# Kernel tuning notes

Hardware: AMD Instinct MI355X
Metric: run time of the kernel (lower is better)

The kernel has to match this reference:

```python
import jax, jax.numpy as jnp
import numpy as np

H = W = 20
NVARS = 4          # n_predictor_vars
NK = 12            # n_conv2d_kernels
NF = NK + NVARS + 1  # 17 augmented channels (conv + original + time)
SIGLEN = NF + NF * NF  # 306, depth-2 signature length
T_END = 1.0        # self.T in the module


def setup_inputs() -> dict:
    key = jax.random.key(0)
    ks = jax.random.split(key, 8)
    B, T = 64, 96
    x = jax.random.normal(ks[0], (B, T, NVARS, H, W), dtype=jnp.float32)
    conv_w = jax.random.normal(ks[1], (NK, NVARS, 3, 3), dtype=jnp.float32) * 0.1
    conv_b = jax.random.normal(ks[2], (NK,), dtype=jnp.float32) * 0.01
    d_in = SIGLEN * H * W  # 122400

    def lin(k, fan_in, fan_out):
        return jax.random.normal(k, (fan_in, fan_out), dtype=jnp.float32) / np.float32(np.sqrt(fan_in))

    w1, b1 = lin(ks[3], d_in, 32), jnp.zeros((32,), jnp.float32)
    w2, b2 = lin(ks[4], 32, 32), jnp.zeros((32,), jnp.float32)
    w3, b3 = lin(ks[5], 32, 32), jnp.zeros((32,), jnp.float32)
    w4, b4 = lin(ks[6], 32, 1), jnp.zeros((1,), jnp.float32)
    return {"x": x, "conv_w": conv_w, "conv_b": conv_b,
            "w1": w1, "b1": b1, "w2": w2, "b2": b2,
            "w3": w3, "b3": b3, "w4": w4, "b4": b4}


def reference(x, conv_w, conv_b, w1, b1, w2, b2, w3, b3, w4, b4):
    B, T = x.shape[0], x.shape[1]
    # Batched conv over all timesteps at once (the torch code loops over t).
    xi = x.reshape(B * T, NVARS, H, W)
    y = jax.lax.conv_general_dilated(
        xi, conv_w, window_strides=(1, 1), padding='SAME',
        dimension_numbers=('NCHW', 'OIHW', 'NCHW'))
    y = y + conv_b[None, :, None, None]
    y = y.reshape(B, T, NK, H, W)
    # Dropout3d is identity in eval mode.
    # Augment: [conv features, original values, time channel] along channel dim.
    tch = jnp.linspace(0.0, T_END, T, dtype=x.dtype).reshape(1, T, 1, 1, 1)
    tch = jnp.broadcast_to(tch, (B, T, 1, H, W))
    feat = jnp.concatenate([y, x, tch], axis=2)        # (B, T, NF, H, W)
    path = jnp.transpose(feat, (0, 3, 4, 1, 2))        # (B, H, W, T, NF)
    # Depth-2 path signature (Chen closed form):
    # level1 = sum dx; level2 = sum_{i<j} dx_i (x) dx_j + 0.5 sum_i dx_i (x) dx_i
    dx = path[..., 1:, :] - path[..., :-1, :]          # (B,H,W,T-1,NF)
    csum = jnp.cumsum(dx, axis=-2)                     # inclusive prefix sums
    lvl1 = csum[..., -1, :]                            # (B,H,W,NF)
    # (exclusive prefix) + 0.5*dx = csum - 0.5*dx -> single contracted einsum
    lvl2 = jnp.einsum('bhwti,bhwtj->bhwij', csum - 0.5 * dx, dx)
    sig = jnp.concatenate([lvl1, lvl2.reshape(B, H, W, NF * NF)], axis=-1)  # (B,H,W,306)
    flat = sig.reshape(B, H * W * SIGLEN)
    h = jax.nn.relu(flat @ w1 + b1)
    h = jax.nn.relu(h @ w2 + b2)
    h = jax.nn.relu(h @ w3 + b3)
    return h @ w4 + b4                                 # (B, 1)
```

## Files before the change

### kernel.cpp

```cpp
#include <hip/hip_runtime.h>

#define HH 20
#define WW 20
#define TT 96
#define BB 64
#define SIG 306
#define NFC 17
#define TSTRIDE 264
#define CHUNK 16
#define NCHUNK 6
#define XT 199
#define KTOT 122400
#define KSLAB 120
#define NSLAB 4
#define NKBLK 255
#define LDT 66

typedef float float4u __attribute__((ext_vector_type(4), aligned(4)));

__global__ __launch_bounds__(256) void sig_kernel(
    const float* __restrict__ x,
    const float* __restrict__ cw,
    float* __restrict__ sig)
{
  __shared__ __align__(16) float feat[15 * TSTRIDE + 256 + 8];
  __shared__ __align__(16) float xs[CHUNK * XT];
  __shared__ __align__(16) float wlds[12 * 48];

  const int tid = threadIdx.x;
  const int blk = blockIdx.x;
  const int b = blk / 25;
  const int tile = blk % 25;
  const int th4 = (tile / 5) * 4, tw4 = (tile % 5) * 4;
  const float* xb0 = x + (size_t)b * TT * 1600;

  #pragma unroll
  for (int r = 0; r < 3; r++) {
    int idx = r * 256 + tid;
    if (idx < 576) {
      int k = idx / 48, rem = idx % 48;
      int ci = rem / 12, r2 = rem % 12, dy = r2 >> 2, dx = r2 & 3;
      wlds[idx] = (dx < 3) ? cw[k * 36 + ci * 9 + dy * 3 + dx] : 0.f;
    }
  }

  int g_off[9], l_off[9];
  #pragma unroll
  for (int r = 0; r < 9; r++) {
    int idx = r * 256 + tid;
    int t = idx / 144, q = idx % 144;
    int ci = q / 36, pos = q % 36, row = pos / 6, col = pos % 6;
    int gr = th4 - 1 + row, gc = tw4 - 1 + col;
    bool valid = (gr >= 0 && gr < HH && gc >= 0 && gc < WW);
    g_off[r] = valid ? (t * 1600 + ci * 400 + gr * WW + gc) : -1;
    l_off[r] = t * XT + ci * 48 + row * 8 + col;
  }

  const int cpix = tid >> 4, ctt = tid & 15;
  const int cpy = cpix >> 2, cpx = cpix & 3;

  const int p2 = tid >> 4;
  const int rr = tid & 15, it = rr >> 2, jt = rr & 3;
  const int i0 = it * 4, j0 = jt * 4;

  float accv[4][4];
  float f0a[4], f0b[4], pa[4], pb[4], fsum[4];
  #pragma unroll
  for (int i = 0; i < 4; i++) {
    #pragma unroll
    for (int j = 0; j < 4; j++) accv[i][j] = 0.f;
  }

  auto stage = [&](int chunk) {
    const float* xbc = xb0 + (size_t)chunk * CHUNK * 1600;
    float rg[9];
    #pragma unroll
    for (int r = 0; r < 9; r++)
      rg[r] = (g_off[r] >= 0) ? xbc[g_off[r]] : 0.f;
    #pragma unroll
    for (int r = 0; r < 9; r++) xs[l_off[r]] = rg[r];
  };

  auto conv = [&]() {
    float win[4][9];
    const int wb2 = ctt * XT;
    #pragma unroll
    for (int ci = 0; ci < 4; ci++)
      #pragma unroll
      for (int dy = 0; dy < 3; dy++)
        #pragma unroll
        for (int dxx = 0; dxx < 3; dxx++)
          win[ci][dy * 3 + dxx] = xs[wb2 + ci * 48 + (cpy + dy) * 8 + (cpx + dxx)];

    float fk[12];
    #pragma unroll
    for (int k = 0; k < 12; k++) {
      float a = 0.f;
      #pragma unroll
      for (int ci = 0; ci < 4; ci++) {
        #pragma unroll
        for (int dy = 0; dy < 3; dy++) {
          const float4 w4 = *reinterpret_cast<const float4*>(
              &wlds[k * 48 + ci * 12 + dy * 4]);
          a += win[ci][dy * 3 + 0] * w4.x + win[ci][dy * 3 + 1] * w4.y +
               win[ci][dy * 3 + 2] * w4.z;
        }
      }
      fk[k] = a;
    }
    float* fr = &feat[ctt * TSTRIDE + cpix * 16];
    *reinterpret_cast<float4*>(fr + 0)  = make_float4(fk[0], fk[1], fk[2], fk[3]);
    *reinterpret_cast<float4*>(fr + 4)  = make_float4(fk[4], fk[5], fk[6], fk[7]);
    *reinterpret_cast<float4*>(fr + 8)  = make_float4(fk[8], fk[9], fk[10], fk[11]);
    *reinterpret_cast<float4*>(fr + 12) = make_float4(win[0][4], win[1][4], win[2][4], win[3][4]);
  };

  auto p2step = [&](int tt) {
    const float* row = &feat[tt * TSTRIDE + p2 * 16];
    const float4 a4 = *reinterpret_cast<const float4*>(row + i0);
    const float4 b4 = *reinterpret_cast<const float4*>(row + j0);
    float fa[4] = {a4.x, a4.y, a4.z, a4.w};
    float fb[4] = {b4.x, b4.y, b4.z, b4.w};
    float sa[4], db[4];
    #pragma unroll
    for (int i = 0; i < 4; i++) { sa[i] = fa[i] + pa[i]; db[i] = fb[i] - pb[i]; }
    #pragma unroll
    for (int i = 0; i < 4; i++)
      #pragma unroll
      for (int j = 0; j < 4; j++) accv[i][j] += sa[i] * db[j];
    #pragma unroll
    for (int i = 0; i < 4; i++) { fsum[i] += fa[i]; pa[i] = fa[i]; pb[i] = fb[i]; }
  };

  stage(0);
  __syncthreads();
  conv();
  __syncthreads();
  {
    const float* r0 = &feat[p2 * 16];
    const float4 a4 = *reinterpret_cast<const float4*>(r0 + i0);
    const float4 b4 = *reinterpret_cast<const float4*>(r0 + j0);
    f0a[0] = a4.x; f0a[1] = a4.y; f0a[2] = a4.z; f0a[3] = a4.w;
    f0b[0] = b4.x; f0b[1] = b4.y; f0b[2] = b4.z; f0b[3] = b4.w;
    #pragma unroll
    for (int i = 0; i < 4; i++) { pa[i] = f0a[i]; pb[i] = f0b[i]; fsum[i] = f0a[i]; }
  }
  #pragma unroll
  for (int tt = 1; tt < CHUNK; tt++) p2step(tt);

  for (int chunk = 1; chunk < NCHUNK; chunk++) {
    __syncthreads();
    stage(chunk);
    __syncthreads();
    conv();
    __syncthreads();
    #pragma unroll
    for (int tt = 0; tt < CHUNK; tt++) p2step(tt);
  }

  {
    const int ph = th4 + (p2 >> 2), pw = tw4 + (p2 & 3);
    float* sb = sig + (size_t)b * KTOT + (size_t)(ph * WW + pw) * SIG;
    float lv1b[4];
    #pragma unroll
    for (int j = 0; j < 4; j++) lv1b[j] = pb[j] - f0b[j];
    #pragma unroll
    for (int ii = 0; ii < 4; ii++) {
      float4u v;
      #pragma unroll
      for (int jj = 0; jj < 4; jj++)
        v[jj] = 0.5f * accv[ii][jj] - f0a[ii] * lv1b[jj];
      *reinterpret_cast<float4u*>(sb + NFC + (i0 + ii) * NFC + j0) = v;
    }
    if (jt == 0) {
      #pragma unroll
      for (int ii = 0; ii < 4; ii++) {
        const int c = i0 + ii;
        const float f0 = f0a[ii], f95 = pa[ii], fs = fsum[ii];
        sb[c] = f95 - f0;
        sb[NFC + c * NFC + 16] = (fs - 95.5f * f0 - 0.5f * f95) * (1.f / 95.f);
        sb[NFC + 16 * NFC + c] = (95.5f * f95 + 0.5f * f0 - fs) * (1.f / 95.f);
      }
      if (it == 0) { sb[16] = 1.0f; sb[NFC + 16 * NFC + 16] = 0.5f; }
    }
  }
}

template<bool ATOMIC>
__global__ __launch_bounds__(256) void mlp1_gemm(
    const float* __restrict__ sig, const float* __restrict__ w1,
    float* __restrict__ part)
{
  __shared__ __align__(16) float ldsT[KSLAB * LDT];
  __shared__ __align__(16) float wls[KSLAB * 32];
  const int tid = threadIdx.x;
  const int n = tid & 31, bq = tid >> 5;
  const int k0 = blockIdx.x * (KSLAB * NSLAB);

  float a8[8];
  #pragma unroll
  for (int i = 0; i < 8; i++) a8[i] = 0.f;

  for (int s = 0; s < NSLAB; s++) {
    const int ks = k0 + s * KSLAB;
    __syncthreads();
    #pragma unroll
    for (int r = 0; r < 30; r++) {
      int idx = r * 256 + tid;
      int b = idx / KSLAB, kk = idx % KSLAB;
      ldsT[kk * LDT + b] = sig[(size_t)b * KTOT + ks + kk];
    }
    #pragma unroll
    for (int r = 0; r < 15; r++) {
      int idx = r * 256 + tid;
      wls[idx] = w1[(size_t)ks * 32 + idx];
    }
    __syncthreads();

    #pragma unroll 4
    for (int kk = 0; kk < KSLAB; kk++) {
      const float w = wls[kk * 32 + n];
      const float4 s0 = *reinterpret_cast<const float4*>(&ldsT[kk * LDT + bq * 8]);
      const float4 s1 = *reinterpret_cast<const float4*>(&ldsT[kk * LDT + bq * 8 + 4]);
      a8[0] += s0.x * w; a8[1] += s0.y * w; a8[2] += s0.z * w; a8[3] += s0.w * w;
      a8[4] += s1.x * w; a8[5] += s1.y * w; a8[6] += s1.z * w; a8[7] += s1.w * w;
    }
  }

  if (ATOMIC) {
    #pragma unroll
    for (int i = 0; i < 8; i++)
      atomicAdd(&part[(bq * 8 + i) * 32 + n], a8[i]);
  } else {
    const size_t pb = (size_t)blockIdx.x * (BB * 32);
    #pragma unroll
    for (int i = 0; i < 8; i++)
      part[pb + (bq * 8 + i) * 32 + n] = a8[i];
  }
}

__global__ __launch_bounds__(256) void mlp_tail(
    const float* __restrict__ part, int npart, const float* __restrict__ b1,
    const float* __restrict__ w2, const float* __restrict__ b2,
    const float* __restrict__ w3, const float* __restrict__ b3,
    const float* __restrict__ w4, const float* __restrict__ b4,
    float* __restrict__ out)
{
  __shared__ float red[8][33];
  const int tid = threadIdx.x;
  const int n = tid & 31;
  const int s = tid >> 5;
  const int b = blockIdx.x;

  float sum = 0.f;
  #pragma unroll 8
  for (int p = s; p < npart; p += 8)
    sum += part[(size_t)p * (BB * 32) + b * 32 + n];
  red[s][n] = sum;
  __syncthreads();

  if (tid < 32) {
    float acc = red[0][n];
    #pragma unroll
    for (int q = 1; q < 8; q++) acc += red[q][n];

    float h = fmaxf(acc + b1[n], 0.f);

    float v = b2[n];
    #pragma unroll
    for (int k = 0; k < 32; k++)
      v += __shfl(h, k, 64) * w2[k * 32 + n];
    h = fmaxf(v, 0.f);

    v = b3[n];
    #pragma unroll
    for (int k = 0; k < 32; k++)
      v += __shfl(h, k, 64) * w3[k * 32 + n];
    h = fmaxf(v, 0.f);

    float p = h * w4[n];
    #pragma unroll
    for (int o = 16; o >= 1; o >>= 1) p += __shfl_xor(p, o, 64);
    if (n == 0) out[b] = p + b4[0];
  }
}

extern "C" void kernel_launch(void* const* d_in, const int* in_sizes, int n_in,
                              void* d_out, int out_size, void* d_ws, size_t ws_size,
                              hipStream_t stream) {
  const float* x  = (const float*)d_in[0];
  const float* cw = (const float*)d_in[1];
  const float* w1 = (const float*)d_in[3];
  const float* b1 = (const float*)d_in[4];
  const float* w2 = (const float*)d_in[5];
  const float* b2 = (const float*)d_in[6];
  const float* w3 = (const float*)d_in[7];
  const float* b3 = (const float*)d_in[8];
  const float* w4 = (const float*)d_in[9];
  const float* b4 = (const float*)d_in[10];
  float* out = (float*)d_out;

  const size_t sig_bytes  = (size_t)BB * KTOT * sizeof(float);
  const size_t part_bytes = (size_t)NKBLK * BB * 32 * sizeof(float);
  float* sigm = (float*)d_ws;

  sig_kernel<<<dim3(1600), dim3(256), 0, stream>>>(x, cw, sigm);

  if (ws_size >= sig_bytes + part_bytes) {
    float* part = (float*)((char*)d_ws + sig_bytes);
    mlp1_gemm<false><<<dim3(NKBLK), dim3(256), 0, stream>>>(sigm, w1, part);
    mlp_tail<<<dim3(64), dim3(256), 0, stream>>>(part, NKBLK, b1, w2, b2, w3, b3, w4, b4, out);
  } else {
    float* acc = (float*)((char*)d_ws + sig_bytes);
    hipMemsetAsync(acc, 0, BB * 32 * sizeof(float), stream);
    mlp1_gemm<true><<<dim3(NKBLK), dim3(256), 0, stream>>>(sigm, w1, acc);
    mlp_tail<<<dim3(64), dim3(256), 0, stream>>>(acc, 1, b1, w2, b2, w3, b3, w4, b4, out);
  }
}
```

Measured before the change: 250.7 us.

## Fuse first MLP layer into signature kernel and retile by batch group

The signature kernel now multiplies each computed signature entry directly by the matching w1 rows and reduces into a 64x32 accumulator with wave shuffles and atomics. This removes the 31MB signature round-trip through global memory and the separate GEMM pass. Blocks are retiled to cover a 2x2 pixel tile for 4 batches, so w1 rows are shared across those batches. In exchange there are many more per-thread global w1 loads (32 floats per signature element), 32 shuffle reductions per thread, and heavy atomic traffic on a small buffer, and the atomics make the summation order nondeterministic.

```diff
diff --git a/kernel.cpp b/kernel.cpp
--- a/kernel.cpp
+++ b/kernel.cpp
@@ -9,30 +9,26 @@
 #define TSTRIDE 264
 #define CHUNK 16
 #define NCHUNK 6
-#define XT 199
-#define KTOT 122400
-#define KSLAB 120
-#define NSLAB 4
-#define NKBLK 255
-#define LDT 66
+#define XTS 65
+#define XBS (CHUNK * XTS)
 
 typedef float float4u __attribute__((ext_vector_type(4), aligned(4)));
 
-__global__ __launch_bounds__(256) void sig_kernel(
+__global__ __launch_bounds__(256) void sig_fused(
     const float* __restrict__ x,
     const float* __restrict__ cw,
-    float* __restrict__ sig)
+    const float* __restrict__ w1,
+    float* __restrict__ acc)
 {
-  __shared__ __align__(16) float feat[15 * TSTRIDE + 256 + 8];
-  __shared__ __align__(16) float xs[CHUNK * XT];
+  __shared__ __align__(16) float feat[CHUNK * TSTRIDE];
+  __shared__ __align__(16) float xs[4 * XBS];
   __shared__ __align__(16) float wlds[12 * 48];
 
   const int tid = threadIdx.x;
   const int blk = blockIdx.x;
-  const int b = blk / 25;
-  const int tile = blk % 25;
-  const int th4 = (tile / 5) * 4, tw4 = (tile % 5) * 4;
-  const float* xb0 = x + (size_t)b * TT * 1600;
+  const int tile = blk >> 4;
+  const int bg   = blk & 15;
+  const int th2 = (tile / 10) * 2, tw2 = (tile % 10) * 2;
 
   #pragma unroll
   for (int r = 0; r < 3; r++) {
@@ -44,53 +40,60 @@
     }
   }
 
-  int g_off[9], l_off[9];
-  #pragma unroll
-  for (int r = 0; r < 9; r++) {
-    int idx = r * 256 + tid;
-    int t = idx / 144, q = idx % 144;
-    int ci = q / 36, pos = q % 36, row = pos / 6, col = pos % 6;
-    int gr = th4 - 1 + row, gc = tw4 - 1 + col;
+  int goff[4], loff[4];
+  #pragma unroll
+  for (int rr = 0; rr < 4; rr++) {
+    int inner = rr * 256 + tid;
+    int t = inner >> 6, s2 = inner & 63;
+    int ci = s2 >> 4, pos = s2 & 15;
+    int pr = pos >> 2, pc = pos & 3;
+    int gr = th2 - 1 + pr, gc = tw2 - 1 + pc;
     bool valid = (gr >= 0 && gr < HH && gc >= 0 && gc < WW);
-    g_off[r] = valid ? (t * 1600 + ci * 400 + gr * WW + gc) : -1;
-    l_off[r] = t * XT + ci * 48 + row * 8 + col;
-  }
-
-  const int cpix = tid >> 4, ctt = tid & 15;
-  const int cpy = cpix >> 2, cpx = cpix & 3;
-
-  const int p2 = tid >> 4;
-  const int rr = tid & 15, it = rr >> 2, jt = rr & 3;
+    goff[rr] = valid ? (t * 1600 + ci * 400 + gr * WW + gc) : -1;
+    loff[rr] = t * XTS + ci * 16 + pos;
+  }
+
+  const int bl  = tid >> 6;
+  const int pix = (tid >> 4) & 3;
+  const int ctt = tid & 15;
+  const int cpy = pix >> 1, cpx = pix & 1;
+  const int rr2 = tid & 15, it = rr2 >> 2, jt = rr2 & 3;
   const int i0 = it * 4, j0 = jt * 4;
 
   float accv[4][4];
   float f0a[4], f0b[4], pa[4], pb[4], fsum[4];
   #pragma unroll
-  for (int i = 0; i < 4; i++) {
+  for (int i = 0; i < 4; i++)
     #pragma unroll
     for (int j = 0; j < 4; j++) accv[i][j] = 0.f;
-  }
 
   auto stage = [&](int chunk) {
-    const float* xbc = xb0 + (size_t)chunk * CHUNK * 1600;
-    float rg[9];
-    #pragma unroll
-    for (int r = 0; r < 9; r++)
-      rg[r] = (g_off[r] >= 0) ? xbc[g_off[r]] : 0.f;
-    #pragma unroll
-    for (int r = 0; r < 9; r++) xs[l_off[r]] = rg[r];
+    const float* xc = x + (size_t)chunk * CHUNK * 1600;
+    float rg[16];
+    #pragma unroll
+    for (int bb = 0; bb < 4; bb++) {
+      const float* xbp = xc + (size_t)(bg * 4 + bb) * TT * 1600;
+      #pragma unroll
+      for (int rr = 0; rr < 4; rr++)
+        rg[bb * 4 + rr] = (goff[rr] >= 0) ? xbp[goff[rr]] : 0.f;
+    }
+    #pragma unroll
+    for (int bb = 0; bb < 4; bb++)
+      #pragma unroll
+      for (int rr = 0; rr < 4; rr++)
+        xs[bb * XBS + loff[rr]] = rg[bb * 4 + rr];
   };
 
   auto conv = [&]() {
     float win[4][9];
-    const int wb2 = ctt * XT;
+    const int wb2 = bl * XBS + ctt * XTS;
     #pragma unroll
     for (int ci = 0; ci < 4; ci++)
       #pragma unroll
       for (int dy = 0; dy < 3; dy++)
         #pragma unroll
         for (int dxx = 0; dxx < 3; dxx++)
-          win[ci][dy * 3 + dxx] = xs[wb2 + ci * 48 + (cpy + dy) * 8 + (cpx + dxx)];
+          win[ci][dy * 3 + dxx] = xs[wb2 + ci * 16 + (cpy + dy) * 4 + (cpx + dxx)];
 
     float fk[12];
     #pragma unroll
@@ -108,7 +111,7 @@
       }
       fk[k] = a;
     }
-    float* fr = &feat[ctt * TSTRIDE + cpix * 16];
+    float* fr = &feat[ctt * TSTRIDE + bl * 64 + pix * 16];
     *reinterpret_cast<float4*>(fr + 0)  = make_float4(fk[0], fk[1], fk[2], fk[3]);
     *reinterpret_cast<float4*>(fr + 4)  = make_float4(fk[4], fk[5], fk[6], fk[7]);
     *reinterpret_cast<float4*>(fr + 8)  = make_float4(fk[8], fk[9], fk[10], fk[11]);
@@ -116,7 +119,7 @@
   };
 
   auto p2step = [&](int tt) {
-    const float* row = &feat[tt * TSTRIDE + p2 * 16];
+    const float* row = &feat[tt * TSTRIDE + bl * 64 + pix * 16];
     const float4 a4 = *reinterpret_cast<const float4*>(row + i0);
     const float4 b4 = *reinterpret_cast<const float4*>(row + j0);
     float fa[4] = {a4.x, a4.y, a4.z, a4.w};
@@ -137,7 +140,7 @@
   conv();
   __syncthreads();
   {
-    const float* r0 = &feat[p2 * 16];
+    const float* r0 = &feat[bl * 64 + pix * 16];
     const float4 a4 = *reinterpret_cast<const float4*>(r0 + i0);
     const float4 b4 = *reinterpret_cast<const float4*>(r0 + j0);
     f0a[0] = a4.x; f0a[1] = a4.y; f0a[2] = a4.z; f0a[3] = a4.w;
@@ -158,131 +161,90 @@
     for (int tt = 0; tt < CHUNK; tt++) p2step(tt);
   }
 
+  float mlp[32];
+  #pragma unroll
+  for (int n = 0; n < 32; n++) mlp[n] = 0.f;
+
   {
-    const int ph = th4 + (p2 >> 2), pw = tw4 + (p2 & 3);
-    float* sb = sig + (size_t)b * KTOT + (size_t)(ph * WW + pw) * SIG;
+    const int pg = (th2 + (pix >> 1)) * WW + (tw2 + (pix & 1));
+    const float* wb1 = w1 + (size_t)pg * SIG * 32;
+
+    auto fma_row = [&](int row, float sv) {
+      const float4* wp = reinterpret_cast<const float4*>(wb1 + (size_t)row * 32);
+      #pragma unroll
+      for (int q = 0; q < 8; q++) {
+        float4 w = wp[q];
+        mlp[q * 4 + 0] += sv * w.x; mlp[q * 4 + 1] += sv * w.y;
+        mlp[q * 4 + 2] += sv * w.z; mlp[q * 4 + 3] += sv * w.w;
+      }
+    };
+
     float lv1b[4];
     #pragma unroll
     for (int j = 0; j < 4; j++) lv1b[j] = pb[j] - f0b[j];
-    #pragma unroll
-    for (int ii = 0; ii < 4; ii++) {
-      float4u v;
+
+    #pragma unroll
+    for (int ii = 0; ii < 4; ii++)
       #pragma unroll
       for (int jj = 0; jj < 4; jj++)
-        v[jj] = 0.5f * accv[ii][jj] - f0a[ii] * lv1b[jj];
-      *reinterpret_cast<float4u*>(sb + NFC + (i0 + ii) * NFC + j0) = v;
-    }
+        fma_row(NFC + (i0 + ii) * NFC + (j0 + jj),
+                0.5f * accv[ii][jj] - f0a[ii] * lv1b[jj]);
+
     if (jt == 0) {
       #pragma unroll
       for (int ii = 0; ii < 4; ii++) {
         const int c = i0 + ii;
         const float f0 = f0a[ii], f95 = pa[ii], fs = fsum[ii];
-        sb[c] = f95 - f0;
-        sb[NFC + c * NFC + 16] = (fs - 95.5f * f0 - 0.5f * f95) * (1.f / 95.f);
-        sb[NFC + 16 * NFC + c] = (95.5f * f95 + 0.5f * f0 - fs) * (1.f / 95.f);
-      }
-      if (it == 0) { sb[16] = 1.0f; sb[NFC + 16 * NFC + 16] = 0.5f; }
-    }
+        fma_row(c, f95 - f0);
+        fma_row(NFC + c * NFC + 16, (fs - 95.5f * f0 - 0.5f * f95) * (1.f / 95.f));
+        fma_row(NFC + 16 * NFC + c, (95.5f * f95 + 0.5f * f0 - fs) * (1.f / 95.f));
+      }
+      if (it == 0) {
+        fma_row(16, 1.0f);
+        fma_row(NFC + 16 * NFC + 16, 0.5f);
+      }
+    }
+  }
+
+  const int bglob = bg * 4 + bl;
+  #pragma unroll
+  for (int n = 0; n < 32; n++) {
+    float v = mlp[n];
+    #pragma unroll
+    for (int o = 32; o >= 1; o >>= 1) v += __shfl_xor(v, o, 64);
+    if ((tid & 63) == 0) atomicAdd(&acc[bglob * 32 + n], v);
   }
 }
 
-template<bool ATOMIC>
-__global__ __launch_bounds__(256) void mlp1_gemm(
-    const float* __restrict__ sig, const float* __restrict__ w1,
-    float* __restrict__ part)
-{
-  __shared__ __align__(16) float ldsT[KSLAB * LDT];
-  __shared__ __align__(16) float wls[KSLAB * 32];
-  const int tid = threadIdx.x;
-  const int n = tid & 31, bq = tid >> 5;
-  const int k0 = blockIdx.x * (KSLAB * NSLAB);
-
-  float a8[8];
-  #pragma unroll
-  for (int i = 0; i < 8; i++) a8[i] = 0.f;
-
-  for (int s = 0; s < NSLAB; s++) {
-    const int ks = k0 + s * KSLAB;
-    __syncthreads();
-    #pragma unroll
-    for (int r = 0; r < 30; r++) {
-      int idx = r * 256 + tid;
-      int b = idx / KSLAB, kk = idx % KSLAB;
-      ldsT[kk * LDT + b] = sig[(size_t)b * KTOT + ks + kk];
-    }
-    #pragma unroll
-    for (int r = 0; r < 15; r++) {
-      int idx = r * 256 + tid;
-      wls[idx] = w1[(size_t)ks * 32 + idx];
-    }
-    __syncthreads();
-
-    #pragma unroll 4
-    for (int kk = 0; kk < KSLAB; kk++) {
-      const float w = wls[kk * 32 + n];
-      const float4 s0 = *reinterpret_cast<const float4*>(&ldsT[kk * LDT + bq * 8]);
-      const float4 s1 = *reinterpret_cast<const float4*>(&ldsT[kk * LDT + bq * 8 + 4]);
-      a8[0] += s0.x * w; a8[1] += s0.y * w; a8[2] += s0.z * w; a8[3] += s0.w * w;
-      a8[4] += s1.x * w; a8[5] += s1.y * w; a8[6] += s1.z * w; a8[7] += s1.w * w;
-    }
-  }
-
-  if (ATOMIC) {
-    #pragma unroll
-    for (int i = 0; i < 8; i++)
-      atomicAdd(&part[(bq * 8 + i) * 32 + n], a8[i]);
-  } else {
-    const size_t pb = (size_t)blockIdx.x * (BB * 32);
-    #pragma unroll
-    for (int i = 0; i < 8; i++)
-      part[pb + (bq * 8 + i) * 32 + n] = a8[i];
-  }
-}
-
-__global__ __launch_bounds__(256) void mlp_tail(
-    const float* __restrict__ part, int npart, const float* __restrict__ b1,
+__global__ __launch_bounds__(64) void mlp_tail(
+    const float* __restrict__ acc, const float* __restrict__ b1,
     const float* __restrict__ w2, const float* __restrict__ b2,
     const float* __restrict__ w3, const float* __restrict__ b3,
     const float* __restrict__ w4, const float* __restrict__ b4,
     float* __restrict__ out)
 {
-  __shared__ float red[8][33];
-  const int tid = threadIdx.x;
-  const int n = tid & 31;
-  const int s = tid >> 5;
+  const int n = threadIdx.x & 31;
   const int b = blockIdx.x;
-
-  float sum = 0.f;
-  #pragma unroll 8
-  for (int p = s; p < npart; p += 8)
-    sum += part[(size_t)p * (BB * 32) + b * 32 + n];
-  red[s][n] = sum;
-  __syncthreads();
-
-  if (tid < 32) {
-    float acc = red[0][n];
-    #pragma unroll
-    for (int q = 1; q < 8; q++) acc += red[q][n];
-
-    float h = fmaxf(acc + b1[n], 0.f);
-
-    float v = b2[n];
-    #pragma unroll
-    for (int k = 0; k < 32; k++)
-      v += __shfl(h, k, 64) * w2[k * 32 + n];
-    h = fmaxf(v, 0.f);
-
-    v = b3[n];
-    #pragma unroll
-    for (int k = 0; k < 32; k++)
-      v += __shfl(h, k, 64) * w3[k * 32 + n];
-    h = fmaxf(v, 0.f);
-
-    float p = h * w4[n];
-    #pragma unroll
-    for (int o = 16; o >= 1; o >>= 1) p += __shfl_xor(p, o, 64);
-    if (n == 0) out[b] = p + b4[0];
-  }
+  if (threadIdx.x >= 32) return;
+
+  float h = fmaxf(acc[b * 32 + n] + b1[n], 0.f);
+
+  float v = b2[n];
+  #pragma unroll
+  for (int k = 0; k < 32; k++)
+    v += __shfl(h, k, 64) * w2[k * 32 + n];
+  h = fmaxf(v, 0.f);
+
+  v = b3[n];
+  #pragma unroll
+  for (int k = 0; k < 32; k++)
+    v += __shfl(h, k, 64) * w3[k * 32 + n];
+  h = fmaxf(v, 0.f);
+
+  float p = h * w4[n];
+  #pragma unroll
+  for (int o = 16; o >= 1; o >>= 1) p += __shfl_xor(p, o, 64);
+  if (n == 0) out[b] = p + b4[0];
 }
 
 extern "C" void kernel_launch(void* const* d_in, const int* in_sizes, int n_in,
@@ -299,21 +261,9 @@
   const float* w4 = (const float*)d_in[9];
   const float* b4 = (const float*)d_in[10];
   float* out = (float*)d_out;
-
-  const size_t sig_bytes  = (size_t)BB * KTOT * sizeof(float);
-  const size_t part_bytes = (size_t)NKBLK * BB * 32 * sizeof(float);
-  float* sigm = (float*)d_ws;
-
-  sig_kernel<<<dim3(1600), dim3(256), 0, stream>>>(x, cw, sigm);
-
-  if (ws_size >= sig_bytes + part_bytes) {
-    float* part = (float*)((char*)d_ws + sig_bytes);
-    mlp1_gemm<false><<<dim3(NKBLK), dim3(256), 0, stream>>>(sigm, w1, part);
-    mlp_tail<<<dim3(64), dim3(256), 0, stream>>>(part, NKBLK, b1, w2, b2, w3, b3, w4, b4, out);
-  } else {
-    float* acc = (float*)((char*)d_ws + sig_bytes);
-    hipMemsetAsync(acc, 0, BB * 32 * sizeof(float), stream);
-    mlp1_gemm<true><<<dim3(NKBLK), dim3(256), 0, stream>>>(sigm, w1, acc);
-    mlp_tail<<<dim3(64), dim3(256), 0, stream>>>(acc, 1, b1, w2, b2, w3, b3, w4, b4, out);
-  }
+  float* acc = (float*)d_ws;
+
+  hipMemsetAsync(acc, 0, BB * 32 * sizeof(float), stream);
+  sig_fused<<<dim3(1600), dim3(256), 0, stream>>>(x, cw, w1, acc);
+  mlp_tail<<<dim3(64), dim3(64), 0, stream>>>(acc, b1, w2, b2, w3, b3, w4, b4, out);
 }
```

Measured after the change: 500.4 us. 2x slower.

## Split first MLP GEMM into more K-blocks with 2x4 register tiles and transposed partials

Applied to the files above, without the earlier changes.

Raises the first-layer GEMM grid from 255 to 1020 K-blocks of one 120-wide slab each, so more of the GPU's compute units have work during this pass over the large weight matrix. Each thread now computes a 2-output by 4-batch tile and reads w1 straight from global as float2 instead of staging it in LDS. Partial sums are stored transposed (output-major, block index contiguous), so the tail kernel can reduce them with contiguous float4 loads. The cost is a larger partials buffer and more reduction work in the tail. The atomic fallback is replaced by a 4-slab configuration that also writes partials, which needs a workspace big enough for 255 partial sets.

```diff
diff --git a/kernel.cpp b/kernel.cpp
--- a/kernel.cpp
+++ b/kernel.cpp
@@ -11,10 +11,7 @@
 #define NCHUNK 6
 #define XT 199
 #define KTOT 122400
-#define KSLAB 120
-#define NSLAB 4
-#define NKBLK 255
-#define LDT 66
+#define LDT 68
 
 typedef float float4u __attribute__((ext_vector_type(4), aligned(4)));
 
@@ -186,61 +183,54 @@
   }
 }
 
-template<bool ATOMIC>
-__global__ __launch_bounds__(256) void mlp1_gemm(
+__global__ __launch_bounds__(256) void mlp1_gemm2(
     const float* __restrict__ sig, const float* __restrict__ w1,
-    float* __restrict__ part)
+    float* __restrict__ part, int nslab, int pstride)
 {
-  __shared__ __align__(16) float ldsT[KSLAB * LDT];
-  __shared__ __align__(16) float wls[KSLAB * 32];
+  __shared__ __align__(16) float ldsT[120 * LDT];
   const int tid = threadIdx.x;
-  const int n = tid & 31, bq = tid >> 5;
-  const int k0 = blockIdx.x * (KSLAB * NSLAB);
-
-  float a8[8];
-  #pragma unroll
-  for (int i = 0; i < 8; i++) a8[i] = 0.f;
-
-  for (int s = 0; s < NSLAB; s++) {
-    const int ks = k0 + s * KSLAB;
-    __syncthreads();
+  const int np = tid & 15;
+  const int bq = tid >> 4;
+
+  float a2[2][4];
+  #pragma unroll
+  for (int j = 0; j < 2; j++)
+    #pragma unroll
+    for (int i = 0; i < 4; i++) a2[j][i] = 0.f;
+
+  for (int s = 0; s < nslab; s++) {
+    const int k0 = (blockIdx.x * nslab + s) * 120;
+    if (s) __syncthreads();
     #pragma unroll
     for (int r = 0; r < 30; r++) {
       int idx = r * 256 + tid;
-      int b = idx / KSLAB, kk = idx % KSLAB;
-      ldsT[kk * LDT + b] = sig[(size_t)b * KTOT + ks + kk];
-    }
-    #pragma unroll
-    for (int r = 0; r < 15; r++) {
-      int idx = r * 256 + tid;
-      wls[idx] = w1[(size_t)ks * 32 + idx];
+      int b = idx / 120, kk = idx % 120;
+      ldsT[kk * LDT + b] = sig[(size_t)b * KTOT + k0 + kk];
     }
     __syncthreads();
 
-    #pragma unroll 4
-    for (int kk = 0; kk < KSLAB; kk++) {
-      const float w = wls[kk * 32 + n];
-      const float4 s0 = *reinterpret_cast<const float4*>(&ldsT[kk * LDT + bq * 8]);
-      const float4 s1 = *reinterpret_cast<const float4*>(&ldsT[kk * LDT + bq * 8 + 4]);
-      a8[0] += s0.x * w; a8[1] += s0.y * w; a8[2] += s0.z * w; a8[3] += s0.w * w;
-      a8[4] += s1.x * w; a8[5] += s1.y * w; a8[6] += s1.z * w; a8[7] += s1.w * w;
-    }
-  }
-
-  if (ATOMIC) {
-    #pragma unroll
-    for (int i = 0; i < 8; i++)
-      atomicAdd(&part[(bq * 8 + i) * 32 + n], a8[i]);
-  } else {
-    const size_t pb = (size_t)blockIdx.x * (BB * 32);
-    #pragma unroll
-    for (int i = 0; i < 8; i++)
-      part[pb + (bq * 8 + i) * 32 + n] = a8[i];
-  }
+    const float* w1p = w1 + (size_t)k0 * 32 + np * 2;
+    #pragma unroll 8
+    for (int kk = 0; kk < 120; kk++) {
+      const float2 w = *reinterpret_cast<const float2*>(w1p + (size_t)kk * 32);
+      const float4 sv = *reinterpret_cast<const float4*>(&ldsT[kk * LDT + bq * 4]);
+      a2[0][0] += w.x * sv.x; a2[0][1] += w.x * sv.y;
+      a2[0][2] += w.x * sv.z; a2[0][3] += w.x * sv.w;
+      a2[1][0] += w.y * sv.x; a2[1][1] += w.y * sv.y;
+      a2[1][2] += w.y * sv.z; a2[1][3] += w.y * sv.w;
+    }
+  }
+
+  #pragma unroll
+  for (int j = 0; j < 2; j++)
+    #pragma unroll
+    for (int i = 0; i < 4; i++)
+      part[(size_t)((bq * 4 + i) * 32 + np * 2 + j) * pstride + blockIdx.x] = a2[j][i];
 }
 
-__global__ __launch_bounds__(256) void mlp_tail(
-    const float* __restrict__ part, int npart, const float* __restrict__ b1,
+__global__ __launch_bounds__(256) void mlp_tail2(
+    const float* __restrict__ part, int nkb, int pstride,
+    const float* __restrict__ b1,
     const float* __restrict__ w2, const float* __restrict__ b2,
     const float* __restrict__ w3, const float* __restrict__ b3,
     const float* __restrict__ w4, const float* __restrict__ b4,
@@ -252,10 +242,19 @@
   const int s = tid >> 5;
   const int b = blockIdx.x;
 
+  const float* pp = part + (size_t)(b * 32 + n) * pstride;
+  const int seg = (nkb + 7) >> 3;
+  const int k0 = s * seg;
+  const int k1 = (k0 + seg < nkb) ? (k0 + seg) : nkb;
+
   float sum = 0.f;
-  #pragma unroll 8
-  for (int p = s; p < npart; p += 8)
-    sum += part[(size_t)p * (BB * 32) + b * 32 + n];
+  int k = k0;
+  #pragma unroll 4
+  for (; k + 3 < k1; k += 4) {
+    const float4 v = *reinterpret_cast<const float4*>(pp + k);
+    sum += v.x + v.y + v.z + v.w;
+  }
+  for (; k < k1; k++) sum += pp[k];
   red[s][n] = sum;
   __syncthreads();
 
@@ -268,14 +267,14 @@
 
     float v = b2[n];
     #pragma unroll
-    for (int k = 0; k < 32; k++)
-      v += __shfl(h, k, 64) * w2[k * 32 + n];
+    for (int k2 = 0; k2 < 32; k2++)
+      v += __shfl(h, k2, 64) * w2[k2 * 32 + n];
     h = fmaxf(v, 0.f);
 
     v = b3[n];
     #pragma unroll
-    for (int k = 0; k < 32; k++)
-      v += __shfl(h, k, 64) * w3[k * 32 + n];
+    for (int k2 = 0; k2 < 32; k2++)
+      v += __shfl(h, k2, 64) * w3[k2 * 32 + n];
     h = fmaxf(v, 0.f);
 
     float p = h * w4[n];
@@ -300,20 +299,19 @@
   const float* b4 = (const float*)d_in[10];
   float* out = (float*)d_out;
 
-  const size_t sig_bytes  = (size_t)BB * KTOT * sizeof(float);
-  const size_t part_bytes = (size_t)NKBLK * BB * 32 * sizeof(float);
+  const size_t sig_bytes = (size_t)BB * KTOT * sizeof(float);
   float* sigm = (float*)d_ws;
+  float* part = (float*)((char*)d_ws + sig_bytes);
+
+  int nkb, nslab, pstride;
+  if (ws_size >= sig_bytes + (size_t)BB * 32 * 1024 * sizeof(float)) {
+    nkb = 1020; nslab = 1; pstride = 1024;
+  } else {
+    nkb = 255;  nslab = 4; pstride = 256;
+  }
 
   sig_kernel<<<dim3(1600), dim3(256), 0, stream>>>(x, cw, sigm);
-
-  if (ws_size >= sig_bytes + part_bytes) {
-    float* part = (float*)((char*)d_ws + sig_bytes);
-    mlp1_gemm<false><<<dim3(NKBLK), dim3(256), 0, stream>>>(sigm, w1, part);
-    mlp_tail<<<dim3(64), dim3(256), 0, stream>>>(part, NKBLK, b1, w2, b2, w3, b3, w4, b4, out);
-  } else {
-    float* acc = (float*)((char*)d_ws + sig_bytes);
-    hipMemsetAsync(acc, 0, BB * 32 * sizeof(float), stream);
-    mlp1_gemm<true><<<dim3(NKBLK), dim3(256), 0, stream>>>(sigm, w1, acc);
-    mlp_tail<<<dim3(64), dim3(256), 0, stream>>>(acc, 1, b1, w2, b2, w3, b3, w4, b4, out);
-  }
+  mlp1_gemm2<<<dim3(nkb), dim3(256), 0, stream>>>(sigm, w1, part, nslab, pstride);
+  mlp_tail2<<<dim3(64), dim3(256), 0, stream>>>(part, nkb, pstride,
+                                                b1, w2, b2, w3, b3, w4, b4, out);
 }
```

Result: slower. 264.7 us (+5.6%).
